# Kernel tuning notes

Hardware: AMD Instinct MI355X
Metric: run time of the kernel (lower is better)

## Reference

```python
import jax, jax.numpy as jnp
import numpy as np

N = 50000
IN_DIM, HID_DIM, OUT_DIM = 512, 256, 64
E = 800000


def setup_inputs() -> dict:
    key = jax.random.key(0)
    k1, k2, k3, k4, k5, k6 = jax.random.split(key, 6)
    x = jax.random.normal(k1, (N, IN_DIM), dtype=jnp.float32)
    edge_index = jax.random.randint(k2, (2, E), 0, N, dtype=jnp.int64)
    # GCNConv parameters (glorot-ish scale)
    W1 = jax.random.normal(k3, (IN_DIM, HID_DIM), dtype=jnp.float32) * (1.0 / np.sqrt(IN_DIM))
    b1 = jnp.zeros((HID_DIM,), dtype=jnp.float32)
    W2 = jax.random.normal(k4, (HID_DIM, OUT_DIM), dtype=jnp.float32) * (1.0 / np.sqrt(HID_DIM))
    b2 = jnp.zeros((OUT_DIM,), dtype=jnp.float32)
    return {"x": x, "W1": W1, "b1": b1, "W2": W2, "b2": b2, "edge_index": edge_index}


def _gcn_conv(x, W, b, src, dst, norm, n_nodes):
    # PyG GCNConv: out[dst] = sum_e norm_e * (x @ W)[src_e] + b
    h = x @ W                              # [N, out]
    msg = h[src] * norm[:, None]           # [E+N, out] gather + scale
    out = jax.ops.segment_sum(msg, dst, num_segments=n_nodes)  # scatter-add
    return out + b


def reference(x, W1, b1, W2, b2, edge_index):
    n = x.shape[0]
    # add self-loops (PyG default add_self_loops=True)
    loop = jnp.arange(n, dtype=edge_index.dtype)
    src = jnp.concatenate([edge_index[0], loop])
    dst = jnp.concatenate([edge_index[1], loop])
    # symmetric normalization: deg computed on destination (in-degree incl. self-loop)
    deg = jax.ops.segment_sum(jnp.ones_like(dst, dtype=x.dtype), dst, num_segments=n)
    dis = jnp.where(deg > 0, jax.lax.rsqrt(jnp.maximum(deg, 1.0)), 0.0)
    norm = dis[src] * dis[dst]
    h = _gcn_conv(x, W1, b1, src, dst, norm, n)
    h = jax.nn.relu(h)
    out = _gcn_conv(h, W2, b2, src, dst, norm, n)
    return out
```

## Files before the change

kernel.cpp:

```cpp
#include <hip/hip_runtime.h>
#include <hip/hip_bf16.h>
#include <hip/hip_fp16.h>
#include <stdint.h>

typedef _Float16 half8_t __attribute__((ext_vector_type(8)));
typedef float f32x4_t __attribute__((ext_vector_type(4)));


__global__ void detect_i64_kernel(const int* __restrict__ idx, int* __restrict__ flag) {
    int t = threadIdx.x;
    int v = idx[2 * t + 1];
    unsigned long long b = __ballot(v == 0);
    if (t == 0) *flag = (b == 0xFFFFFFFFFFFFFFFFULL) ? 1 : 0;
}

__device__ __forceinline__ int load_idx(const int* __restrict__ idx, long long pos, int is64) {
    return is64 ? idx[2 * pos] : idx[pos];
}

#define EPB 4096

__global__ __launch_bounds__(256) void bin_count_kernel(
        const int* __restrict__ idx, const int* __restrict__ flag,
        int* __restrict__ bcnt, int E, int N) {
    __shared__ int hist[256];
    hist[threadIdx.x] = 0;
    __syncthreads();
    const int is64 = *flag;
    const int base = blockIdx.x * EPB;
    const int cnt = (E - base < EPB) ? E - base : EPB;
    for (int i = threadIdx.x; i < cnt; i += 256) {
        int d = load_idx(idx, (long long)E + base + i, is64);
        if ((unsigned)d < (unsigned)N) atomicAdd(&hist[d >> 8], 1);
    }
    __syncthreads();
    int h = hist[threadIdx.x];
    if (h) atomicAdd(&bcnt[threadIdx.x], h);
}

__global__ __launch_bounds__(256) void scan_buckets_kernel(
        const int* __restrict__ bcnt, int* __restrict__ bbase,
        int* __restrict__ bcur, int NB) {
    __shared__ int buf[256];
    int t = threadIdx.x;
    int v = (t < NB) ? bcnt[t] : 0;
    buf[t] = v;
    __syncthreads();
    #pragma unroll
    for (int off = 1; off < 256; off <<= 1) {
        int u = (t >= off) ? buf[t - off] : 0;
        __syncthreads();
        buf[t] += u;
        __syncthreads();
    }
    int excl = buf[t] - v;
    if (t < NB) { bbase[t] = excl; bcur[t] = excl; }
    if (t == NB - 1) bbase[NB] = buf[t];
}

__global__ __launch_bounds__(256) void bin_scatter_kernel(
        const int* __restrict__ idx, const int* __restrict__ flag,
        int* __restrict__ bcur, unsigned* __restrict__ packed, int E, int N) {
    __shared__ int cur[256];
    cur[threadIdx.x] = 0;
    __syncthreads();
    const int is64 = *flag;
    const int base = blockIdx.x * EPB;
    const int cnt = (E - base < EPB) ? E - base : EPB;
    for (int i = threadIdx.x; i < cnt; i += 256) {
        int d = load_idx(idx, (long long)E + base + i, is64);
        if ((unsigned)d < (unsigned)N) atomicAdd(&cur[d >> 8], 1);
    }
    __syncthreads();
    int h = cur[threadIdx.x];
    int bs = h ? atomicAdd(&bcur[threadIdx.x], h) : 0;
    __syncthreads();
    cur[threadIdx.x] = bs;
    __syncthreads();
    for (int i = threadIdx.x; i < cnt; i += 256) {
        int d = load_idx(idx, (long long)E + base + i, is64);
        if ((unsigned)d >= (unsigned)N) continue;
        int s = load_idx(idx, base + i, is64);
        if ((unsigned)s >= (unsigned)N) s = 0;
        int pos = atomicAdd(&cur[d >> 8], 1);
        packed[pos] = (unsigned)s | ((unsigned)(d & 255) << 16);
    }
}

__global__ __launch_bounds__(256) void bucket_sort_kernel(
        const unsigned* __restrict__ packed, const int* __restrict__ bbase,
        int* __restrict__ csr_src, int* __restrict__ offsets,
        float* __restrict__ dis, int N, int NB) {
    __shared__ int buf[256];
    __shared__ int cur[256];
    const int b = blockIdx.x;
    const int t = threadIdx.x;
    cur[t] = 0;
    __syncthreads();
    const int e0 = bbase[b], e1 = bbase[b + 1];
    for (int i = e0 + t; i < e1; i += 256)
        atomicAdd(&cur[(packed[i] >> 16) & 255], 1);
    __syncthreads();
    int v = cur[t];
    buf[t] = v;
    __syncthreads();
    #pragma unroll
    for (int off = 1; off < 256; off <<= 1) {
        int u = (t >= off) ? buf[t - off] : 0;
        __syncthreads();
        buf[t] += u;
        __syncthreads();
    }
    int excl = buf[t] - v;
    cur[t] = excl;
    int node = b * 256 + t;
    if (node < N) {
        offsets[node] = e0 + excl;
        dis[node] = rsqrtf((float)(v + 1));
    }
    if (b == NB - 1 && t == 0) offsets[N] = bbase[NB];
    __syncthreads();
    for (int i = e0 + t; i < e1; i += 256) {
        unsigned rec = packed[i];
        int dl = (rec >> 16) & 255;
        int pos = atomicAdd(&cur[dl], 1);
        csr_src[e0 + pos] = (int)(rec & 0xFFFF);
    }
}

__global__ void wt_kernel(const float* __restrict__ W1, const float* __restrict__ W2,
                          _Float16* __restrict__ w1t, _Float16* __restrict__ w2t) {
    int p = blockIdx.x * 256 + threadIdx.x;
    if (p < 512 * 256) {
        int k = p >> 8, n = p & 255;
        w1t[n * 512 + k] = (_Float16)W1[p];
    } else {
        int q = p - 512 * 256;
        if (q < 256 * 64) {
            int k = q >> 6, n = q & 63;
            w2t[n * 256 + k] = (_Float16)W2[q];
        }
    }
}

__global__ __launch_bounds__(256, 3) void gemm1_kernel(
        const float* __restrict__ x, const _Float16* __restrict__ w1t,
        const float* __restrict__ dis, _Float16* __restrict__ h1s, int M) {
    __shared__ _Float16 As[4 * 65 * 8];
    __shared__ _Float16 Bs[4 * 257 * 8];
    const int tid = threadIdx.x;
    const int brow = blockIdx.x * 64;
    const int w = tid >> 6, lane = tid & 63;
    const int wcol = w * 64;
    const int lrow = lane & 15, lkb = lane >> 4;

    const int arow = tid >> 2, akb = tid & 3;
    const int gr = brow + arow;
    const bool aval = gr < M;
    const float* xptr = x + (size_t)(aval ? gr : 0) * 512 + akb * 8;
    const _Float16* bbase = w1t + (size_t)arow * 512 + akb * 8;
    const int awr = (akb * 65 + arow) << 3;
    const int bwr0 = (akb * 257 + arow) << 3;

    f32x4_t acc[4][4];
    #pragma unroll
    for (int mi = 0; mi < 4; ++mi)
        #pragma unroll
        for (int nj = 0; nj < 4; ++nj) acc[mi][nj] = (f32x4_t)0.f;

    float4 au = make_float4(0.f, 0.f, 0.f, 0.f);
    float4 av = make_float4(0.f, 0.f, 0.f, 0.f);
    half8_t bh0, bh1, bh2, bh3;

    if (aval) { au = *(const float4*)(xptr); av = *(const float4*)(xptr + 4); }
    bh0 = *(const half8_t*)(bbase);
    bh1 = *(const half8_t*)(bbase + 64 * 512);
    bh2 = *(const half8_t*)(bbase + 128 * 512);
    bh3 = *(const half8_t*)(bbase + 192 * 512);

    for (int t = 0; t < 16; ++t) {
        __syncthreads();
        half8_t ha;
        ha[0] = (_Float16)au.x; ha[1] = (_Float16)au.y;
        ha[2] = (_Float16)au.z; ha[3] = (_Float16)au.w;
        ha[4] = (_Float16)av.x; ha[5] = (_Float16)av.y;
        ha[6] = (_Float16)av.z; ha[7] = (_Float16)av.w;
        *(half8_t*)&As[awr] = ha;
        *(half8_t*)&Bs[bwr0] = bh0;
        *(half8_t*)&Bs[bwr0 + 64 * 8] = bh1;
        *(half8_t*)&Bs[bwr0 + 128 * 8] = bh2;
        *(half8_t*)&Bs[bwr0 + 192 * 8] = bh3;
        __syncthreads();
        if (t < 15) {
            int k0 = (t + 1) * 32;
            if (aval) {
                au = *(const float4*)(xptr + k0);
                av = *(const float4*)(xptr + k0 + 4);
            }
            bh0 = *(const half8_t*)(bbase + k0);
            bh1 = *(const half8_t*)(bbase + k0 + 64 * 512);
            bh2 = *(const half8_t*)(bbase + k0 + 128 * 512);
            bh3 = *(const half8_t*)(bbase + k0 + 192 * 512);
        }
        half8_t a[4], b[4];
        #pragma unroll
        for (int mi = 0; mi < 4; ++mi)
            a[mi] = *(const half8_t*)&As[(lkb * 65 + mi * 16 + lrow) << 3];
        #pragma unroll
        for (int nj = 0; nj < 4; ++nj)
            b[nj] = *(const half8_t*)&Bs[(lkb * 257 + wcol + nj * 16 + lrow) << 3];
        #pragma unroll
        for (int mi = 0; mi < 4; ++mi)
            #pragma unroll
            for (int nj = 0; nj < 4; ++nj)
                acc[mi][nj] = __builtin_amdgcn_mfma_f32_16x16x32_f16(a[mi], b[nj], acc[mi][nj], 0, 0, 0);
    }
    #pragma unroll
    for (int mi = 0; mi < 4; ++mi) {
        #pragma unroll
        for (int r = 0; r < 4; ++r) {
            int grow = brow + mi * 16 + (lane >> 4) * 4 + r;
            if (grow >= M) continue;
            float s = dis[grow];
            #pragma unroll
            for (int nj = 0; nj < 4; ++nj) {
                int col = wcol + nj * 16 + lrow;
                h1s[((size_t)(col >> 5) * M + grow) * 32 + (col & 31)] =
                    (_Float16)(acc[mi][nj][r] * s);
            }
        }
    }
}

__global__ __launch_bounds__(256, 4) void gemm2_kernel(
        const _Float16* __restrict__ a1s, const _Float16* __restrict__ w2t,
        const float* __restrict__ dis, _Float16* __restrict__ h2s, int M) {
    __shared__ _Float16 As[4 * 65 * 8];
    __shared__ _Float16 Bs[4 * 65 * 8];
    const int tid = threadIdx.x;
    const int brow = blockIdx.x * 64;
    const int w = tid >> 6, lane = tid & 63;
    const int lrow = lane & 15, lkb = lane >> 4;

    const int arow = tid >> 2, akb = tid & 3;
    const int gr = brow + arow;
    const bool aval = gr < M;
    const _Float16* aptr = a1s + ((size_t)(aval ? gr : 0)) * 32 + akb * 8;
    const _Float16* bptr = w2t + (size_t)arow * 256 + akb * 8;
    const int awr = (akb * 65 + arow) << 3;

    f32x4_t acc[4];
    #pragma unroll
    for (int nj = 0; nj < 4; ++nj) acc[nj] = (f32x4_t)0.f;

    const half8_t zero8 = (half8_t)(_Float16)0.f;
    half8_t ah = zero8, bh;
    if (aval) ah = *(const half8_t*)(aptr);
    bh = *(const half8_t*)(bptr);

    for (int t = 0; t < 8; ++t) {
        __syncthreads();
        *(half8_t*)&As[awr] = ah;
        *(half8_t*)&Bs[awr] = bh;
        __syncthreads();
        if (t < 7) {
            if (aval) ah = *(const half8_t*)(aptr + (size_t)(t + 1) * M * 32);
            bh = *(const half8_t*)(bptr + (t + 1) * 32);
        }
        half8_t a = *(const half8_t*)&As[(lkb * 65 + w * 16 + lrow) << 3];
        half8_t b[4];
        #pragma unroll
        for (int nj = 0; nj < 4; ++nj)
            b[nj] = *(const half8_t*)&Bs[(lkb * 65 + nj * 16 + lrow) << 3];
        #pragma unroll
        for (int nj = 0; nj < 4; ++nj)
            acc[nj] = __builtin_amdgcn_mfma_f32_16x16x32_f16(a, b[nj], acc[nj], 0, 0, 0);
    }
    #pragma unroll
    for (int r = 0; r < 4; ++r) {
        int grow = brow + w * 16 + (lane >> 4) * 4 + r;
        if (grow >= M) continue;
        float s = dis[grow];
        #pragma unroll
        for (int nj = 0; nj < 4; ++nj) {
            int col = nj * 16 + lrow;
            h2s[((size_t)(col >> 5) * M + grow) * 32 + (col & 31)] =
                (_Float16)(acc[nj][r] * s);
        }
    }
}

__device__ __forceinline__ float4 up4(uint2 v) {
    __half2 h0 = *reinterpret_cast<__half2*>(&v.x);
    __half2 h1 = *reinterpret_cast<__half2*>(&v.y);
    float2 a = __half22float2(h0), b = __half22float2(h1);
    return make_float4(a.x, a.y, b.x, b.y);
}

__device__ __forceinline__ uint2 pk2(uint2 a, uint2 b) {
    __half2 ax = *reinterpret_cast<__half2*>(&a.x);
    __half2 ay = *reinterpret_cast<__half2*>(&a.y);
    __half2 bx = *reinterpret_cast<__half2*>(&b.x);
    __half2 by = *reinterpret_cast<__half2*>(&b.y);
    __half2 rx = __hadd2(ax, bx);
    __half2 ry = __hadd2(ay, by);
    uint2 r;
    r.x = *reinterpret_cast<unsigned*>(&rx);
    r.y = *reinterpret_cast<unsigned*>(&ry);
    return r;
}

template<int NCH, int FP16OUT>
__global__ __launch_bounds__(256) void aggv_kernel(
        const _Float16* __restrict__ g, const int* __restrict__ offsets,
        const int* __restrict__ csr_src, const float* __restrict__ dis,
        const float* __restrict__ bias, void* __restrict__ out, int N) {
    constexpr int CAP = 2048;
    __shared__ int lds_csr[CAP];
    const int chunk = blockIdx.x % NCH;
    const int nodeBase = (blockIdx.x / NCH) * 32;
    const int grp = threadIdx.x >> 3;
    const int cl = threadIdx.x & 7;
    const int node = nodeBase + grp;
    const bool active = node < N;
    const int nend = (nodeBase + 32 < N) ? nodeBase + 32 : N;
    const int blk0 = offsets[nodeBase];
    const int blk1 = offsets[nend];
    const uint2* gc = (const uint2*)g + (size_t)chunk * N * 8;

    int gs0 = 0, gs1 = 0;
    float s = 0.f;
    if (active) { gs0 = offsets[node]; gs1 = offsets[node + 1]; s = dis[node]; }

    float4 accA = make_float4(0.f, 0.f, 0.f, 0.f);
    float4 accB = make_float4(0.f, 0.f, 0.f, 0.f);
    if (active) accA = up4(gc[(size_t)node * 8 + cl]);

    for (int base = blk0; base < blk1; base += CAP) {
        const int cnt = (blk1 - base < CAP) ? blk1 - base : CAP;
        __syncthreads();
        for (int i = threadIdx.x; i < cnt; i += 256)
            lds_csr[i] = csr_src[base + i];
        __syncthreads();
        int lo = (gs0 > base ? gs0 : base) - base;
        int hiv = (gs1 < base + cnt ? gs1 : base + cnt) - base;
        int e = lo;
        for (; e + 4 <= hiv; e += 4) {
            int s0 = lds_csr[e], s1 = lds_csr[e + 1];
            int s2 = lds_csr[e + 2], s3 = lds_csr[e + 3];
            uint2 v0 = gc[(size_t)s0 * 8 + cl];
            uint2 v1 = gc[(size_t)s1 * 8 + cl];
            uint2 v2 = gc[(size_t)s2 * 8 + cl];
            uint2 v3 = gc[(size_t)s3 * 8 + cl];
            uint2 q = pk2(pk2(v0, v1), pk2(v2, v3));
            float4 f = up4(q);
            accA.x += f.x; accA.y += f.y; accA.z += f.z; accA.w += f.w;
        }
        for (; e < hiv; ++e) {
            int s0 = lds_csr[e];
            float4 f = up4(gc[(size_t)s0 * 8 + cl]);
            accB.x += f.x; accB.y += f.y; accB.z += f.z; accB.w += f.w;
        }
    }
    if (active) {
        float4 bb = *(const float4*)&bias[chunk * 32 + cl * 4];
        float4 o;
        o.x = fmaf(s, accA.x + accB.x, bb.x);
        o.y = fmaf(s, accA.y + accB.y, bb.y);
        o.z = fmaf(s, accA.z + accB.z, bb.z);
        o.w = fmaf(s, accA.w + accB.w, bb.w);
        if (FP16OUT) {
            o.x = fmaxf(o.x, 0.f); o.y = fmaxf(o.y, 0.f);
            o.z = fmaxf(o.z, 0.f); o.w = fmaxf(o.w, 0.f);
            __half2 p0 = __float22half2_rn(make_float2(o.x, o.y));
            __half2 p1 = __float22half2_rn(make_float2(o.z, o.w));
            uint2 pv;
            pv.x = *reinterpret_cast<unsigned*>(&p0);
            pv.y = *reinterpret_cast<unsigned*>(&p1);
            ((uint2*)out)[((size_t)chunk * N + node) * 8 + cl] = pv;
        } else {
            ((float4*)out)[(size_t)node * (NCH * 8) + chunk * 8 + cl] = o;
        }
    }
}

extern "C" void kernel_launch(void* const* d_in, const int* in_sizes, int n_in,
                              void* d_out, int out_size, void* d_ws, size_t ws_size,
                              hipStream_t stream) {
    const float* x  = (const float*)d_in[0];
    const float* W1 = (const float*)d_in[1];
    const float* b1 = (const float*)d_in[2];
    const float* W2 = (const float*)d_in[3];
    const float* b2 = (const float*)d_in[4];
    const int* eidx = (const int*)d_in[5];

    const int HID = in_sizes[2];
    const int OUT = in_sizes[4];
    const int IN  = in_sizes[1] / HID;
    const int N   = in_sizes[0] / IN;
    const int E   = in_sizes[5] / 2;
    const int NB  = (N + 255) >> 8;

    char* ws = (char*)d_ws;
    size_t off = 0;
    auto alloc = [&](size_t bytes) {
        off = (off + 255) & ~(size_t)255;
        char* p = ws + off;
        off += bytes;
        return p;
    };
    float* dis       = (float*)alloc((size_t)N * 4);
    int* flag        = (int*)alloc(256);
    int* bcnt        = (int*)alloc(256 * 4);
    int* bbase       = (int*)alloc(260 * 4);
    int* bcur        = (int*)alloc(256 * 4);
    int* offsets     = (int*)alloc((size_t)(N + 1) * 4);
    unsigned* packed = (unsigned*)alloc((size_t)E * 4);
    int* csr_src     = (int*)alloc((size_t)E * 4);
    _Float16* w1t    = (_Float16*)alloc((size_t)IN * HID * 2);
    _Float16* w2t    = (_Float16*)alloc((size_t)HID * OUT * 2);
    _Float16* h1s    = (_Float16*)alloc((size_t)N * HID * 2);
    _Float16* a1s    = (_Float16*)alloc((size_t)N * HID * 2);
    _Float16* h2s    = (_Float16*)alloc((size_t)N * OUT * 2);

    const int nblkE = (E + EPB - 1) / EPB;

    hipMemsetAsync(bcnt, 0, 256 * 4, stream);
    detect_i64_kernel<<<1, 64, 0, stream>>>(eidx, flag);
    bin_count_kernel<<<nblkE, 256, 0, stream>>>(eidx, flag, bcnt, E, N);
    scan_buckets_kernel<<<1, 256, 0, stream>>>(bcnt, bbase, bcur, NB);
    bin_scatter_kernel<<<nblkE, 256, 0, stream>>>(eidx, flag, bcur, packed, E, N);
    bucket_sort_kernel<<<NB, 256, 0, stream>>>(packed, bbase, csr_src, offsets, dis, N, NB);
    wt_kernel<<<(IN * HID + HID * OUT + 255) / 256, 256, 0, stream>>>(W1, W2, w1t, w2t);

    gemm1_kernel<<<(N + 63) / 64, 256, 0, stream>>>(x, w1t, dis, h1s, N);
    aggv_kernel<8, 1><<<((N + 31) / 32) * 8, 256, 0, stream>>>(h1s, offsets, csr_src, dis,
                                                               b1, a1s, N);
    gemm2_kernel<<<(N + 63) / 64, 256, 0, stream>>>(a1s, w2t, dis, h2s, N);
    aggv_kernel<2, 0><<<((N + 31) / 32) * 2, 256, 0, stream>>>(h2s, offsets, csr_src, dis,
                                                               b2, d_out, N);
}
```

Baseline: 160.6 us.

## Widen GEMM1 K-tile, use 16-byte gathers in aggregation, fold memset into detect

gemm1 now stages a 64-wide K slice per iteration, with each thread loading one full W1t row segment. That halves the number of barriers and loop iterations at the cost of more LDS and registers under launch_bounds(256,3). The aggregation kernel now has 4 threads per node, each gathering 16-byte uint4 rows and covering 64 nodes per block. This doubles bytes per load instruction and halves the block count. The bcnt memset is folded into the detect kernel to drop one API call.

```diff
diff --git a/kernel.cpp b/kernel.cpp
--- a/kernel.cpp
+++ b/kernel.cpp
@@ -7,11 +7,16 @@
 typedef float f32x4_t __attribute__((ext_vector_type(4)));
 
 
-__global__ void detect_i64_kernel(const int* __restrict__ idx, int* __restrict__ flag) {
+__global__ __launch_bounds__(256) void detect_i64_kernel(const int* __restrict__ idx,
+                                                         int* __restrict__ flag,
+                                                         int* __restrict__ bcnt) {
     int t = threadIdx.x;
-    int v = idx[2 * t + 1];
-    unsigned long long b = __ballot(v == 0);
-    if (t == 0) *flag = (b == 0xFFFFFFFFFFFFFFFFULL) ? 1 : 0;
+    if (t < 64) {
+        int v = idx[2 * t + 1];
+        unsigned long long b = __ballot(v == 0);
+        if (t == 0) *flag = (b == 0xFFFFFFFFFFFFFFFFULL) ? 1 : 0;
+    }
+    bcnt[t] = 0;
 }
 
 __device__ __forceinline__ int load_idx(const int* __restrict__ idx, long long pos, int is64) {
@@ -146,21 +151,21 @@
 __global__ __launch_bounds__(256, 3) void gemm1_kernel(
         const float* __restrict__ x, const _Float16* __restrict__ w1t,
         const float* __restrict__ dis, _Float16* __restrict__ h1s, int M) {
-    __shared__ _Float16 As[4 * 65 * 8];
-    __shared__ _Float16 Bs[4 * 257 * 8];
+    __shared__ _Float16 As[8 * 65 * 8];
+    __shared__ _Float16 Bs[8 * 257 * 8];
     const int tid = threadIdx.x;
     const int brow = blockIdx.x * 64;
     const int w = tid >> 6, lane = tid & 63;
     const int wcol = w * 64;
     const int lrow = lane & 15, lkb = lane >> 4;
 
-    const int arow = tid >> 2, akb = tid & 3;
+    const int arow = tid >> 2, akq = tid & 3;
     const int gr = brow + arow;
     const bool aval = gr < M;
-    const float* xptr = x + (size_t)(aval ? gr : 0) * 512 + akb * 8;
-    const _Float16* bbase = w1t + (size_t)arow * 512 + akb * 8;
-    const int awr = (akb * 65 + arow) << 3;
-    const int bwr0 = (akb * 257 + arow) << 3;
+    const float* xptr = x + (size_t)(aval ? gr : 0) * 512 + akq * 16;
+    const _Float16* bptr = w1t + (size_t)tid * 512;
+    const int awr0 = ((akq * 2) * 65 + arow) << 3;
+    const int awr1 = ((akq * 2 + 1) * 65 + arow) << 3;
 
     f32x4_t acc[4][4];
     #pragma unroll
@@ -168,52 +173,62 @@
         #pragma unroll
         for (int nj = 0; nj < 4; ++nj) acc[mi][nj] = (f32x4_t)0.f;
 
-    float4 au = make_float4(0.f, 0.f, 0.f, 0.f);
-    float4 av = make_float4(0.f, 0.f, 0.f, 0.f);
-    half8_t bh0, bh1, bh2, bh3;
-
-    if (aval) { au = *(const float4*)(xptr); av = *(const float4*)(xptr + 4); }
-    bh0 = *(const half8_t*)(bbase);
-    bh1 = *(const half8_t*)(bbase + 64 * 512);
-    bh2 = *(const half8_t*)(bbase + 128 * 512);
-    bh3 = *(const half8_t*)(bbase + 192 * 512);
-
-    for (int t = 0; t < 16; ++t) {
-        __syncthreads();
-        half8_t ha;
-        ha[0] = (_Float16)au.x; ha[1] = (_Float16)au.y;
-        ha[2] = (_Float16)au.z; ha[3] = (_Float16)au.w;
-        ha[4] = (_Float16)av.x; ha[5] = (_Float16)av.y;
-        ha[6] = (_Float16)av.z; ha[7] = (_Float16)av.w;
-        *(half8_t*)&As[awr] = ha;
-        *(half8_t*)&Bs[bwr0] = bh0;
-        *(half8_t*)&Bs[bwr0 + 64 * 8] = bh1;
-        *(half8_t*)&Bs[bwr0 + 128 * 8] = bh2;
-        *(half8_t*)&Bs[bwr0 + 192 * 8] = bh3;
-        __syncthreads();
-        if (t < 15) {
-            int k0 = (t + 1) * 32;
+    float4 a0 = make_float4(0,0,0,0), a1 = a0, a2 = a0, a3 = a0;
+    half8_t b[8];
+
+    if (aval) {
+        a0 = *(const float4*)(xptr);
+        a1 = *(const float4*)(xptr + 4);
+        a2 = *(const float4*)(xptr + 8);
+        a3 = *(const float4*)(xptr + 12);
+    }
+    #pragma unroll
+    for (int kb = 0; kb < 8; ++kb) b[kb] = *(const half8_t*)(bptr + kb * 8);
+
+    for (int t = 0; t < 8; ++t) {
+        __syncthreads();
+        half8_t h0, h1;
+        h0[0] = (_Float16)a0.x; h0[1] = (_Float16)a0.y;
+        h0[2] = (_Float16)a0.z; h0[3] = (_Float16)a0.w;
+        h0[4] = (_Float16)a1.x; h0[5] = (_Float16)a1.y;
+        h0[6] = (_Float16)a1.z; h0[7] = (_Float16)a1.w;
+        h1[0] = (_Float16)a2.x; h1[1] = (_Float16)a2.y;
+        h1[2] = (_Float16)a2.z; h1[3] = (_Float16)a2.w;
+        h1[4] = (_Float16)a3.x; h1[5] = (_Float16)a3.y;
+        h1[6] = (_Float16)a3.z; h1[7] = (_Float16)a3.w;
+        *(half8_t*)&As[awr0] = h0;
+        *(half8_t*)&As[awr1] = h1;
+        #pragma unroll
+        for (int kb = 0; kb < 8; ++kb)
+            *(half8_t*)&Bs[(kb * 257 + tid) << 3] = b[kb];
+        __syncthreads();
+        if (t < 7) {
+            int k0 = (t + 1) * 64;
             if (aval) {
-                au = *(const float4*)(xptr + k0);
-                av = *(const float4*)(xptr + k0 + 4);
+                a0 = *(const float4*)(xptr + k0);
+                a1 = *(const float4*)(xptr + k0 + 4);
+                a2 = *(const float4*)(xptr + k0 + 8);
+                a3 = *(const float4*)(xptr + k0 + 12);
             }
-            bh0 = *(const half8_t*)(bbase + k0);
-            bh1 = *(const half8_t*)(bbase + k0 + 64 * 512);
-            bh2 = *(const half8_t*)(bbase + k0 + 128 * 512);
-            bh3 = *(const half8_t*)(bbase + k0 + 192 * 512);
-        }
-        half8_t a[4], b[4];
-        #pragma unroll
-        for (int mi = 0; mi < 4; ++mi)
-            a[mi] = *(const half8_t*)&As[(lkb * 65 + mi * 16 + lrow) << 3];
-        #pragma unroll
-        for (int nj = 0; nj < 4; ++nj)
-            b[nj] = *(const half8_t*)&Bs[(lkb * 257 + wcol + nj * 16 + lrow) << 3];
-        #pragma unroll
-        for (int mi = 0; mi < 4; ++mi)
+            #pragma unroll
+            for (int kb = 0; kb < 8; ++kb)
+                b[kb] = *(const half8_t*)(bptr + k0 + kb * 8);
+        }
+        #pragma unroll
+        for (int h = 0; h < 2; ++h) {
+            half8_t af[4], bf[4];
+            #pragma unroll
+            for (int mi = 0; mi < 4; ++mi)
+                af[mi] = *(const half8_t*)&As[((h * 4 + lkb) * 65 + mi * 16 + lrow) << 3];
             #pragma unroll
             for (int nj = 0; nj < 4; ++nj)
-                acc[mi][nj] = __builtin_amdgcn_mfma_f32_16x16x32_f16(a[mi], b[nj], acc[mi][nj], 0, 0, 0);
+                bf[nj] = *(const half8_t*)&Bs[((h * 4 + lkb) * 257 + wcol + nj * 16 + lrow) << 3];
+            #pragma unroll
+            for (int mi = 0; mi < 4; ++mi)
+                #pragma unroll
+                for (int nj = 0; nj < 4; ++nj)
+                    acc[mi][nj] = __builtin_amdgcn_mfma_f32_16x16x32_f16(af[mi], bf[nj], acc[mi][nj], 0, 0, 0);
+        }
     }
     #pragma unroll
     for (int mi = 0; mi < 4; ++mi) {
@@ -297,16 +312,19 @@
     return make_float4(a.x, a.y, b.x, b.y);
 }
 
-__device__ __forceinline__ uint2 pk2(uint2 a, uint2 b) {
-    __half2 ax = *reinterpret_cast<__half2*>(&a.x);
-    __half2 ay = *reinterpret_cast<__half2*>(&a.y);
-    __half2 bx = *reinterpret_cast<__half2*>(&b.x);
-    __half2 by = *reinterpret_cast<__half2*>(&b.y);
-    __half2 rx = __hadd2(ax, bx);
-    __half2 ry = __hadd2(ay, by);
-    uint2 r;
-    r.x = *reinterpret_cast<unsigned*>(&rx);
-    r.y = *reinterpret_cast<unsigned*>(&ry);
+__device__ __forceinline__ unsigned pkw(unsigned a, unsigned b) {
+    __half2 ha = *reinterpret_cast<__half2*>(&a);
+    __half2 hb = *reinterpret_cast<__half2*>(&b);
+    __half2 r = __hadd2(ha, hb);
+    return *reinterpret_cast<unsigned*>(&r);
+}
+
+__device__ __forceinline__ uint4 pk4(uint4 a, uint4 b) {
+    uint4 r;
+    r.x = pkw(a.x, b.x);
+    r.y = pkw(a.y, b.y);
+    r.z = pkw(a.z, b.z);
+    r.w = pkw(a.w, b.w);
     return r;
 }
 
@@ -318,23 +336,29 @@
     constexpr int CAP = 2048;
     __shared__ int lds_csr[CAP];
     const int chunk = blockIdx.x % NCH;
-    const int nodeBase = (blockIdx.x / NCH) * 32;
-    const int grp = threadIdx.x >> 3;
-    const int cl = threadIdx.x & 7;
+    const int nodeBase = (blockIdx.x / NCH) * 64;
+    const int grp = threadIdx.x >> 2;
+    const int cl = threadIdx.x & 3;
     const int node = nodeBase + grp;
     const bool active = node < N;
-    const int nend = (nodeBase + 32 < N) ? nodeBase + 32 : N;
+    const int nend = (nodeBase + 64 < N) ? nodeBase + 64 : N;
     const int blk0 = offsets[nodeBase];
     const int blk1 = offsets[nend];
-    const uint2* gc = (const uint2*)g + (size_t)chunk * N * 8;
+    const uint4* gc = (const uint4*)g + (size_t)chunk * N * 4;
 
     int gs0 = 0, gs1 = 0;
     float s = 0.f;
     if (active) { gs0 = offsets[node]; gs1 = offsets[node + 1]; s = dis[node]; }
 
-    float4 accA = make_float4(0.f, 0.f, 0.f, 0.f);
-    float4 accB = make_float4(0.f, 0.f, 0.f, 0.f);
-    if (active) accA = up4(gc[(size_t)node * 8 + cl]);
+    float4 accLo = make_float4(0.f, 0.f, 0.f, 0.f);
+    float4 accHi = make_float4(0.f, 0.f, 0.f, 0.f);
+    if (active) {
+        uint4 sv = gc[(size_t)node * 4 + cl];
+        float4 lo = up4(make_uint2(sv.x, sv.y));
+        float4 hi = up4(make_uint2(sv.z, sv.w));
+        accLo.x += lo.x; accLo.y += lo.y; accLo.z += lo.z; accLo.w += lo.w;
+        accHi.x += hi.x; accHi.y += hi.y; accHi.z += hi.z; accHi.w += hi.w;
+    }
 
     for (int base = blk0; base < blk1; base += CAP) {
         const int cnt = (blk1 - base < CAP) ? blk1 - base : CAP;
@@ -342,44 +366,61 @@
         for (int i = threadIdx.x; i < cnt; i += 256)
             lds_csr[i] = csr_src[base + i];
         __syncthreads();
-        int lo = (gs0 > base ? gs0 : base) - base;
-        int hiv = (gs1 < base + cnt ? gs1 : base + cnt) - base;
-        int e = lo;
-        for (; e + 4 <= hiv; e += 4) {
+        int lo_e = (gs0 > base ? gs0 : base) - base;
+        int hi_e = (gs1 < base + cnt ? gs1 : base + cnt) - base;
+        int e = lo_e;
+        for (; e + 4 <= hi_e; e += 4) {
             int s0 = lds_csr[e], s1 = lds_csr[e + 1];
             int s2 = lds_csr[e + 2], s3 = lds_csr[e + 3];
-            uint2 v0 = gc[(size_t)s0 * 8 + cl];
-            uint2 v1 = gc[(size_t)s1 * 8 + cl];
-            uint2 v2 = gc[(size_t)s2 * 8 + cl];
-            uint2 v3 = gc[(size_t)s3 * 8 + cl];
-            uint2 q = pk2(pk2(v0, v1), pk2(v2, v3));
-            float4 f = up4(q);
-            accA.x += f.x; accA.y += f.y; accA.z += f.z; accA.w += f.w;
-        }
-        for (; e < hiv; ++e) {
+            uint4 v0 = gc[(size_t)s0 * 4 + cl];
+            uint4 v1 = gc[(size_t)s1 * 4 + cl];
+            uint4 v2 = gc[(size_t)s2 * 4 + cl];
+            uint4 v3 = gc[(size_t)s3 * 4 + cl];
+            uint4 q = pk4(pk4(v0, v1), pk4(v2, v3));
+            float4 flo = up4(make_uint2(q.x, q.y));
+            float4 fhi = up4(make_uint2(q.z, q.w));
+            accLo.x += flo.x; accLo.y += flo.y; accLo.z += flo.z; accLo.w += flo.w;
+            accHi.x += fhi.x; accHi.y += fhi.y; accHi.z += fhi.z; accHi.w += fhi.w;
+        }
+        for (; e < hi_e; ++e) {
             int s0 = lds_csr[e];
-            float4 f = up4(gc[(size_t)s0 * 8 + cl]);
-            accB.x += f.x; accB.y += f.y; accB.z += f.z; accB.w += f.w;
+            uint4 v = gc[(size_t)s0 * 4 + cl];
+            float4 flo = up4(make_uint2(v.x, v.y));
+            float4 fhi = up4(make_uint2(v.z, v.w));
+            accLo.x += flo.x; accLo.y += flo.y; accLo.z += flo.z; accLo.w += flo.w;
+            accHi.x += fhi.x; accHi.y += fhi.y; accHi.z += fhi.z; accHi.w += fhi.w;
         }
     }
     if (active) {
-        float4 bb = *(const float4*)&bias[chunk * 32 + cl * 4];
-        float4 o;
-        o.x = fmaf(s, accA.x + accB.x, bb.x);
-        o.y = fmaf(s, accA.y + accB.y, bb.y);
-        o.z = fmaf(s, accA.z + accB.z, bb.z);
-        o.w = fmaf(s, accA.w + accB.w, bb.w);
+        float4 bb0 = *(const float4*)&bias[chunk * 32 + cl * 8];
+        float4 bb1 = *(const float4*)&bias[chunk * 32 + cl * 8 + 4];
+        float4 o0, o1;
+        o0.x = fmaf(s, accLo.x, bb0.x);
+        o0.y = fmaf(s, accLo.y, bb0.y);
+        o0.z = fmaf(s, accLo.z, bb0.z);
+        o0.w = fmaf(s, accLo.w, bb0.w);
+        o1.x = fmaf(s, accHi.x, bb1.x);
+        o1.y = fmaf(s, accHi.y, bb1.y);
+        o1.z = fmaf(s, accHi.z, bb1.z);
+        o1.w = fmaf(s, accHi.w, bb1.w);
         if (FP16OUT) {
-            o.x = fmaxf(o.x, 0.f); o.y = fmaxf(o.y, 0.f);
-            o.z = fmaxf(o.z, 0.f); o.w = fmaxf(o.w, 0.f);
-            __half2 p0 = __float22half2_rn(make_float2(o.x, o.y));
-            __half2 p1 = __float22half2_rn(make_float2(o.z, o.w));
-            uint2 pv;
+            o0.x = fmaxf(o0.x, 0.f); o0.y = fmaxf(o0.y, 0.f);
+            o0.z = fmaxf(o0.z, 0.f); o0.w = fmaxf(o0.w, 0.f);
+            o1.x = fmaxf(o1.x, 0.f); o1.y = fmaxf(o1.y, 0.f);
+            o1.z = fmaxf(o1.z, 0.f); o1.w = fmaxf(o1.w, 0.f);
+            __half2 p0 = __float22half2_rn(make_float2(o0.x, o0.y));
+            __half2 p1 = __float22half2_rn(make_float2(o0.z, o0.w));
+            __half2 p2 = __float22half2_rn(make_float2(o1.x, o1.y));
+            __half2 p3 = __float22half2_rn(make_float2(o1.z, o1.w));
+            uint4 pv;
             pv.x = *reinterpret_cast<unsigned*>(&p0);
             pv.y = *reinterpret_cast<unsigned*>(&p1);
-            ((uint2*)out)[((size_t)chunk * N + node) * 8 + cl] = pv;
+            pv.z = *reinterpret_cast<unsigned*>(&p2);
+            pv.w = *reinterpret_cast<unsigned*>(&p3);
+            ((uint4*)out)[((size_t)chunk * N + node) * 4 + cl] = pv;
         } else {
-            ((float4*)out)[(size_t)node * (NCH * 8) + chunk * 8 + cl] = o;
+            ((float4*)out)[(size_t)node * (NCH * 8) + chunk * 8 + cl * 2]     = o0;
+            ((float4*)out)[(size_t)node * (NCH * 8) + chunk * 8 + cl * 2 + 1] = o1;
         }
     }
 }
@@ -425,8 +466,7 @@
 
     const int nblkE = (E + EPB - 1) / EPB;
 
-    hipMemsetAsync(bcnt, 0, 256 * 4, stream);
-    detect_i64_kernel<<<1, 64, 0, stream>>>(eidx, flag);
+    detect_i64_kernel<<<1, 256, 0, stream>>>(eidx, flag, bcnt);
     bin_count_kernel<<<nblkE, 256, 0, stream>>>(eidx, flag, bcnt, E, N);
     scan_buckets_kernel<<<1, 256, 0, stream>>>(bcnt, bbase, bcur, NB);
     bin_scatter_kernel<<<nblkE, 256, 0, stream>>>(eidx, flag, bcur, packed, E, N);
@@ -434,9 +474,9 @@
     wt_kernel<<<(IN * HID + HID * OUT + 255) / 256, 256, 0, stream>>>(W1, W2, w1t, w2t);
 
     gemm1_kernel<<<(N + 63) / 64, 256, 0, stream>>>(x, w1t, dis, h1s, N);
-    aggv_kernel<8, 1><<<((N + 31) / 32) * 8, 256, 0, stream>>>(h1s, offsets, csr_src, dis,
+    aggv_kernel<8, 1><<<((N + 63) / 64) * 8, 256, 0, stream>>>(h1s, offsets, csr_src, dis,
                                                                b1, a1s, N);
     gemm2_kernel<<<(N + 63) / 64, 256, 0, stream>>>(a1s, w2t, dis, h2s, N);
-    aggv_kernel<2, 0><<<((N + 31) / 32) * 2, 256, 0, stream>>>(h2s, offsets, csr_src, dis,
+    aggv_kernel<2, 0><<<((N + 63) / 64) * 2, 256, 0, stream>>>(h2s, offsets, csr_src, dis,
                                                                b2, d_out, N);
 }
```

New measurement: 170.4 us. +6.1%, slower.
